# Optimization experiments

Measured on AMD Instinct MI355X. Metric: run time of the kernel, lower is better.

Reference implementation:

```python
import jax, jax.numpy as jnp
import numpy as np

B, N_MELS, T_IN = 4, 80, 2048
N_CTX, E, H, L, M, C = 1024, 768, 12, 6, 3072, 527
HD = E // H  # 64


def _sinusoids(length, channels, max_timescale=10000):
    log_inc = np.log(max_timescale) / (channels // 2 - 1)
    inv = np.exp(-log_inc * np.arange(channels // 2))
    t = np.arange(length)[:, None] * inv[None, :]
    return jnp.asarray(np.concatenate([np.sin(t), np.cos(t)], axis=1), dtype=jnp.float32)


def _ln(x, g, b, eps=1e-5):
    m = jnp.mean(x, axis=-1, keepdims=True)
    v = jnp.mean(jnp.square(x - m), axis=-1, keepdims=True)
    return (x - m) * jax.lax.rsqrt(v + eps) * g + b


def setup_inputs() -> dict:
    key = jax.random.key(0)
    ks = iter(jax.random.split(key, 40))
    s = 0.02
    d = {
        "x": jax.random.normal(next(ks), (B, N_MELS, T_IN), jnp.float32),
        "conv1_w": jax.random.normal(next(ks), (E, N_MELS, 3), jnp.float32) * s,
        "conv1_b": jnp.zeros((E,), jnp.float32),
        "conv2_w": jax.random.normal(next(ks), (E, E, 3), jnp.float32) * s,
        "conv2_b": jnp.zeros((E,), jnp.float32),
        "pos_emb": _sinusoids(N_CTX, E),
        "ln1_g": jnp.ones((L, E), jnp.float32),
        "ln1_b": jnp.zeros((L, E), jnp.float32),
        "wq": jax.random.normal(next(ks), (L, H, E, HD), jnp.float32) * s,
        "bq": jnp.zeros((L, H, HD), jnp.float32),
        "wk": jax.random.normal(next(ks), (L, H, E, HD), jnp.float32) * s,
        "bk": jnp.zeros((L, H, HD), jnp.float32),
        "wv": jax.random.normal(next(ks), (L, H, E, HD), jnp.float32) * s,
        "bv": jnp.zeros((L, H, HD), jnp.float32),
        "wo": jax.random.normal(next(ks), (L, E, E), jnp.float32) * s,
        "bo": jnp.zeros((L, E), jnp.float32),
        "w1": jax.random.normal(next(ks), (L, E, M), jnp.float32) * s,
        "b1": jnp.zeros((L, M), jnp.float32),
        "w2": jax.random.normal(next(ks), (L, M, E), jnp.float32) * s,
        "b2": jnp.zeros((L, E), jnp.float32),
        "ln2_g": jnp.ones((L, E), jnp.float32),
        "ln2_b": jnp.zeros((L, E), jnp.float32),
        "lnp_g": jnp.ones((E,), jnp.float32),
        "lnp_b": jnp.zeros((E,), jnp.float32),
        "hln_g": jnp.ones((E,), jnp.float32),
        "hln_b": jnp.zeros((E,), jnp.float32),
        "hw1": jax.random.normal(next(ks), (E, M), jnp.float32) * s,
        "hb1": jnp.zeros((M,), jnp.float32),
        "hw2": jax.random.normal(next(ks), (M, C), jnp.float32) * s,
        "hb2": jnp.zeros((C,), jnp.float32),
    }
    return d


def reference(x, conv1_w, conv1_b, conv2_w, conv2_b, pos_emb,
              ln1_g, ln1_b, wq, bq, wk, bk, wv, bv, wo, bo,
              w1, b1, w2, b2, ln2_g, ln2_b, lnp_g, lnp_b,
              hln_g, hln_b, hw1, hb1, hw2, hb2):
    # conv stem: (B, n_mels, T) -> (B, E, T) -> (B, E, T/2), exact (erf) GELU
    x = jax.lax.conv_general_dilated(x, conv1_w, (1,), [(1, 1)],
                                     dimension_numbers=("NCH", "OIH", "NCH"))
    x = jax.nn.gelu(x + conv1_b[None, :, None], approximate=False)
    x = jax.lax.conv_general_dilated(x, conv2_w, (2,), [(1, 1)],
                                     dimension_numbers=("NCH", "OIH", "NCH"))
    x = jax.nn.gelu(x + conv2_b[None, :, None], approximate=False)
    x = jnp.transpose(x, (0, 2, 1))  # (B, T, E), T == N_CTX
    x = x + pos_emb[: x.shape[1]]

    b, t, e = x.shape
    for l in range(L):
        # batched per-head QKV (original loops over heads; same math)
        q = jnp.einsum("bte,hed->bhtd", x, wq[l]) + bq[l][None, :, None, :]
        k = jnp.einsum("bte,hed->bhtd", x, wk[l]) + bk[l][None, :, None, :]
        v = jnp.einsum("bte,hed->bhtd", x, wv[l]) + bv[l][None, :, None, :]
        # NOTE: no 1/sqrt(d) scaling in the original module
        a = jax.nn.softmax(jnp.einsum("bhid,bhjd->bhij", q, k), axis=-1)
        hds = jnp.einsum("bhij,bhjd->bhid", a, v)
        concat = jnp.transpose(hds, (0, 2, 1, 3)).reshape(b, t, e)
        attn_out = concat @ wo[l] + bo[l]
        x = _ln(x + attn_out, ln1_g[l], ln1_b[l])
        ffn = jax.nn.relu(x @ w1[l] + b1[l]) @ w2[l] + b2[l]
        x = _ln(ffn + x, ln2_g[l], ln2_b[l])

    x = _ln(x, lnp_g, lnp_b)
    cls = x[:, 0]
    cls = _ln(cls, hln_g, hln_b)
    logits = jax.nn.relu(cls @ hw1 + hb1) @ hw2 + hb2  # dropout inactive (eval)
    return jax.nn.softmax(logits, axis=-1)
```

## Files before the change

kernel.cpp:

```cpp
#include <hip/hip_runtime.h>
#include <hip/hip_bf16.h>

typedef __hip_bfloat16 bf16;
using v8s   = __attribute__((ext_vector_type(8))) short;
using f32x4 = __attribute__((ext_vector_type(4))) float;

#define DI __device__ __forceinline__

DI float gelu_f(float x) { return 0.5f * x * (1.f + erff(x * 0.70710678118654752f)); }

DI void g2lds16(const bf16* g, bf16* l) {
  __builtin_amdgcn_global_load_lds((const __attribute__((address_space(1))) void*)g,
                                   (__attribute__((address_space(3))) void*)l, 16, 0, 0);
}

template<int N> DI void vm_barrier() {
  if constexpr (N == 0)      asm volatile("s_waitcnt vmcnt(0)\ns_barrier" ::: "memory");
  else if constexpr (N == 2) asm volatile("s_waitcnt vmcnt(2)\ns_barrier" ::: "memory");
  else if constexpr (N == 4) asm volatile("s_waitcnt vmcnt(4)\ns_barrier" ::: "memory");
  else if constexpr (N == 6) asm volatile("s_waitcnt vmcnt(6)\ns_barrier" ::: "memory");
  else if constexpr (N == 8) asm volatile("s_waitcnt vmcnt(8)\ns_barrier" ::: "memory");
}
DI void lds_barrier() { asm volatile("s_barrier" ::: "memory"); }

DI float block_sum(float v, float* red, int tid) {
#pragma unroll
  for (int o = 32; o > 0; o >>= 1) v += __shfl_down(v, o);
  __syncthreads();
  if ((tid & 63) == 0) red[tid >> 6] = v;
  __syncthreads();
  return red[0] + red[1] + red[2] + red[3];
}
DI float block_max(float v, float* red, int tid) {
#pragma unroll
  for (int o = 32; o > 0; o >>= 1) v = fmaxf(v, __shfl_down(v, o));
  __syncthreads();
  if ((tid & 63) == 0) red[tid >> 6] = v;
  __syncthreads();
  return fmaxf(fmaxf(red[0], red[1]), fmaxf(red[2], red[3]));
}

__global__ __launch_bounds__(256)
void tconv(const float* __restrict__ in, bf16* __restrict__ out,
           int R, int C, long inStrideZ, long outStrideL, long outStrideH, int zmod) {
  __shared__ float tile[32][33];
  int z = blockIdx.z;
  int lz = z / zmod, hz = z - lz * zmod;
  in  += (long)z * inStrideZ;
  out += (long)lz * outStrideL + (long)hz * outStrideH;
  int cb = blockIdx.x * 32, rb = blockIdx.y * 32;
  int tx = threadIdx.x & 31, ty = threadIdx.x >> 5;
#pragma unroll
  for (int i = 0; i < 32; i += 8)
    tile[ty + i][tx] = in[(long)(rb + ty + i) * C + cb + tx];
  __syncthreads();
#pragma unroll
  for (int i = 0; i < 32; i += 8)
    out[(long)(cb + ty + i) * R + rb + tx] = __float2bfloat16(tile[tx][ty + i]);
}

__global__ __launch_bounds__(256)
void prep_cw(const float* __restrict__ wsrc, bf16* __restrict__ o, int IC, int KT) {
  int idx = blockIdx.x * 256 + threadIdx.x;
  int oc = idx / KT, kp = idx - oc * KT;
  float v = 0.f;
  if (kp < IC * 3) {
    int kk = kp / IC, ic = kp - kk * IC;
    v = wsrc[(oc * IC + ic) * 3 + kk];
  }
  o[idx] = __float2bfloat16(v);
}

__global__ __launch_bounds__(256)
void prep_bias(const float* __restrict__ bq, const float* __restrict__ bk,
               const float* __restrict__ bv, float* __restrict__ o) {
  int idx = blockIdx.x * 256 + threadIdx.x;
  int l = idx / 2304, n = idx - l * 2304;
  int which = n / 768, r = n - which * 768;
  const float* src = which == 0 ? bq : (which == 1 ? bk : bv);
  o[idx] = src[l * 768 + r];
}

__global__ __launch_bounds__(256)
void prep_hw2(const float* __restrict__ hw2, const float* __restrict__ hb2,
              float* __restrict__ hw2p, float* __restrict__ hb2p) {
  int idx = blockIdx.x * 256 + threadIdx.x;
  int e = idx / 640, c = idx - e * 640;
  hw2p[idx] = c < 527 ? hw2[(long)e * 527 + c] : 0.f;
  if (idx < 640) hb2p[idx] = idx < 527 ? hb2[idx] : 0.f;
}

__global__ __launch_bounds__(256)
void im2col1(const float* __restrict__ x, bf16* __restrict__ out) {
  int idx = blockIdx.x * 256 + threadIdx.x;
  int m = idx >> 8, kp = idx & 255;
  float v = 0.f;
  if (kp < 240) {
    int kk = kp / 80, ic = kp - kk * 80;
    int t = (m & 2047) + kk - 1;
    int b = m >> 11;
    if ((unsigned)t < 2048u) v = x[((long)(b * 80 + ic) << 11) + t];
  }
  out[idx] = __float2bfloat16(v);
}

__global__ __launch_bounds__(256)
void im2col2(const bf16* __restrict__ y, bf16* __restrict__ out) {
  int idx = blockIdx.x * 256 + threadIdx.x;
  int m = idx / 2304, kp = idx - m * 2304;
  int kk = kp / 768, ic = kp - kk * 768;
  int t = 2 * (m & 1023) + kk - 1;
  bf16 v = __float2bfloat16(0.f);
  if ((unsigned)t < 2048u) v = y[((long)(m >> 10) * 2048 + t) * 768 + ic];
  out[idx] = v;
}

enum { EPI_GELU_BF16, EPI_CONV2, EPI_QKV, EPI_BIAS_F32, EPI_RELU_BF16 };

struct GP {
  const bf16* A; const bf16* B; const float* bias;
  bf16* Ob; float* Of; const float* aux;
  int M, N, K; long sA, sB, sC; int zoff;
};

template<int BM, int BN, int WM, int WN, int EPI, int DBUF>
__global__ __launch_bounds__(WM * WN * 64, 2)
void gemm_bt(GP p) {
  constexpr int WAVES = WM * WN;
  constexpr int FM = BM / WM / 16, FN = BN / WN / 16;
  constexpr int LDN = BM / 8 / WAVES + BN / 8 / WAVES;
  __shared__ __align__(16) bf16 As0[BM * 64], Bs0[BN * 64];
  __shared__ __align__(16) bf16 As1[DBUF ? BM * 64 : 8], Bs1[DBUF ? BN * 64 : 8];
  const int tid = threadIdx.x;
  const int lane = tid & 63, wid = tid >> 6;
  const int wr = wid / WN, wc = wid - wr * WN;
  const int row0 = wr * (BM / WM), col0 = wc * (BN / WN);
  const int lr = lane & 15, lk = (lane >> 4) * 8;
  const int lrow = lane >> 3;
  const int scol = (((lane & 7) ^ (lane >> 3)) & 7) * 8;
  const int rswz = (lr & 7) * 8;
  const int z = blockIdx.z;
  const bf16* Ab = p.A + (long)z * p.sA + (long)blockIdx.x * BM * p.K;
  const bf16* Bb = p.B + (long)z * p.sB + (long)blockIdx.y * BN * p.K;
  f32x4 acc[FM][FN] = {};

  auto stage = [&](bf16* As, bf16* Bs, int kt) {
#pragma unroll
    for (int i = 0; i < BM / 8 / WAVES; ++i) {
      const int c = wid + i * WAVES;
      g2lds16(&Ab[(long)(c * 8 + lrow) * p.K + kt + scol], &As[c << 9]);
    }
#pragma unroll
    for (int i = 0; i < BN / 8 / WAVES; ++i) {
      const int c = wid + i * WAVES;
      g2lds16(&Bb[(long)(c * 8 + lrow) * p.K + kt + scol], &Bs[c << 9]);
    }
  };

  auto compute = [&](const bf16* As, const bf16* Bs) {
#pragma unroll
    for (int ks = 0; ks < 2; ++ks) {
      v8s af[FM], bf_[FN];
#pragma unroll
      for (int mi = 0; mi < FM; ++mi)
        af[mi] = *(const v8s*)&As[(row0 + mi * 16 + lr) * 64 + ((ks * 32 + lk) ^ rswz)];
#pragma unroll
      for (int ni = 0; ni < FN; ++ni)
        bf_[ni] = *(const v8s*)&Bs[(col0 + ni * 16 + lr) * 64 + ((ks * 32 + lk) ^ rswz)];
      __builtin_amdgcn_s_setprio(1);
#pragma unroll
      for (int mi = 0; mi < FM; ++mi)
#pragma unroll
        for (int ni = 0; ni < FN; ++ni)
          acc[mi][ni] = __builtin_amdgcn_mfma_f32_16x16x32_bf16(af[mi], bf_[ni], acc[mi][ni], 0, 0, 0);
      __builtin_amdgcn_s_setprio(0);
    }
  };

  if constexpr (DBUF) {
    stage(As0, Bs0, 0);
    int kt = 0;
    while (true) {
      bool more = kt + 64 < p.K;
      if (more) { stage(As1, Bs1, kt + 64); vm_barrier<LDN>(); } else vm_barrier<0>();
      compute(As0, Bs0);
      kt += 64;
      if (kt >= p.K) break;
      lds_barrier();
      more = kt + 64 < p.K;
      if (more) { stage(As0, Bs0, kt + 64); vm_barrier<LDN>(); } else vm_barrier<0>();
      compute(As1, Bs1);
      kt += 64;
      if (kt >= p.K) break;
      lds_barrier();
    }
  } else {
    for (int kt = 0; kt < p.K; kt += 64) {
      __syncthreads();
      stage(As0, Bs0, kt);
      __syncthreads();
      compute(As0, Bs0);
    }
  }

#pragma unroll
  for (int mi = 0; mi < FM; ++mi) {
#pragma unroll
    for (int ni = 0; ni < FN; ++ni) {
#pragma unroll
      for (int r = 0; r < 4; ++r) {
        float v = acc[mi][ni][r];
        const int m = blockIdx.x * BM + row0 + mi * 16 + (lane >> 4) * 4 + r;
        const int n = blockIdx.y * BN + col0 + ni * 16 + lr;
        if constexpr (EPI == EPI_GELU_BF16) {
          p.Ob[(long)m * p.N + n] = __float2bfloat16(gelu_f(v + p.bias[n]));
        } else if constexpr (EPI == EPI_CONV2) {
          float t = gelu_f(v + p.bias[n]) + p.aux[(long)(m & 1023) * 768 + n];
          p.Of[(long)m * 768 + n] = t;
          p.Ob[(long)m * 768 + n] = __float2bfloat16(t);
        } else if constexpr (EPI == EPI_QKV) {
          float t = v + p.bias[n];
          int which = n / 768, nn = n - which * 768;
          int h = nn >> 6, d = nn & 63;
          long bh = (long)(m >> 10) * 12 + h;
          if (which < 2)
            p.Ob[(long)which * 3145728 + (bh << 16) + ((long)(m & 1023) << 6) + d] = __float2bfloat16(t);
          else
            p.Ob[6291456L + (bh << 16) + ((long)d << 10) + (m & 1023)] = __float2bfloat16(t);
        } else if constexpr (EPI == EPI_BIAS_F32) {
          p.Of[(long)m * p.N + n] = v + p.bias[n];
        } else if constexpr (EPI == EPI_RELU_BF16) {
          p.Ob[(long)m * p.N + n] = __float2bfloat16(fmaxf(v + p.bias[n], 0.f));
        }
      }
    }
  }
}

__global__ __launch_bounds__(256)
void attn_flash(const bf16* __restrict__ qkv, bf16* __restrict__ cc) {
  __shared__ __align__(16) bf16 Ks[2][64 * 64], Vs[2][64 * 64];
  __shared__ __align__(16) bf16 Pl[4][16 * 64];
  const int tid = threadIdx.x, lane = tid & 63, wid = tid >> 6;
  const int lr = lane & 15, lg = lane >> 4;
  const int blk = blockIdx.x;
  const int qt = blk / 48, bh = blk - qt * 48;
  const int b = bh / 12, h = bh - b * 12;
  const long qb = (long)bh << 16;
  const bf16* Qg = qkv + qb;
  const bf16* Kg = qkv + 3145728 + qb;
  const bf16* Vg = qkv + 6291456 + qb;
  const int q0 = qt * 64 + wid * 16;
  const int lrow8 = lane >> 3;
  const int scol = (((lane & 7) ^ (lane >> 3)) & 7) * 8;
  const int rswz = (lr & 7) * 8;

  v8s aq[2];
#pragma unroll
  for (int ks = 0; ks < 2; ++ks)
    aq[ks] = *(const v8s*)&Qg[(long)(q0 + lr) * 64 + ks * 32 + lg * 8];

  const short oneb = (short)0x3F80;
  const v8s ones = {oneb, oneb, oneb, oneb, oneb, oneb, oneb, oneb};

  float mrow[4] = {-1e30f, -1e30f, -1e30f, -1e30f};
  f32x4 acc[4] = {};
  f32x4 lacc = {};
  bf16* myP = &Pl[wid][0];

  auto stageKV = [&](int buf, int kt) {
#pragma unroll
    for (int i = 0; i < 2; ++i) {
      int c = wid + i * 4;
      g2lds16(&Kg[(long)(kt + c * 8 + lrow8) * 64 + scol], &Ks[buf][c << 9]);
      g2lds16(&Vg[((long)(c * 8 + lrow8) << 10) + kt + scol], &Vs[buf][c << 9]);
    }
  };

  stageKV(0, 0);

  for (int it = 0; it < 16; ++it) {
    const int cur = it & 1;
    if (it + 1 < 16) { stageKV(cur ^ 1, (it + 1) * 64); vm_barrier<4>(); }
    else vm_barrier<0>();
    const bf16* Kc = &Ks[cur][0];
    const bf16* Vc = &Vs[cur][0];

    f32x4 s[4] = {};
#pragma unroll
    for (int ks = 0; ks < 2; ++ks) {
      v8s bk[4];
#pragma unroll
      for (int ni = 0; ni < 4; ++ni)
        bk[ni] = *(const v8s*)&Kc[(ni * 16 + lr) * 64 + ((ks * 32 + lg * 8) ^ rswz)];
      __builtin_amdgcn_s_setprio(1);
#pragma unroll
      for (int ni = 0; ni < 4; ++ni)
        s[ni] = __builtin_amdgcn_mfma_f32_16x16x32_bf16(aq[ks], bk[ni], s[ni], 0, 0, 0);
      __builtin_amdgcn_s_setprio(0);
    }

    float tloc[4];
    bool need = false;
#pragma unroll
    for (int r = 0; r < 4; ++r) {
      tloc[r] = fmaxf(fmaxf(s[0][r], s[1][r]), fmaxf(s[2][r], s[3][r]));
      need = need || (tloc[r] > mrow[r] + 8.f);
    }
    if (__any(need)) {
#pragma unroll
      for (int r = 0; r < 4; ++r) {
        float t = tloc[r];
#pragma unroll
        for (int o = 1; o < 16; o <<= 1) t = fmaxf(t, __shfl_xor(t, o));
        float mn = fmaxf(mrow[r], t);
        float al = __expf(mrow[r] - mn);
        mrow[r] = mn;
        lacc[r] *= al;
#pragma unroll
        for (int ni = 0; ni < 4; ++ni) acc[ni][r] *= al;
      }
    }
#pragma unroll
    for (int r = 0; r < 4; ++r) {
      const int row = lg * 4 + r;
      const int prow = row * 64, psw = (row & 7) * 8;
#pragma unroll
      for (int ni = 0; ni < 4; ++ni)
        myP[prow + ((ni * 16 + lr) ^ psw)] = __float2bfloat16(__expf(s[ni][r] - mrow[r]));
    }

#pragma unroll
    for (int ks = 0; ks < 2; ++ks) {
      v8s pa, bv[4];
      pa = *(const v8s*)&myP[lr * 64 + ((ks * 32 + lg * 8) ^ ((lr & 7) * 8))];
#pragma unroll
      for (int ni = 0; ni < 4; ++ni)
        bv[ni] = *(const v8s*)&Vc[(ni * 16 + lr) * 64 + ((ks * 32 + lg * 8) ^ rswz)];
      __builtin_amdgcn_s_setprio(1);
#pragma unroll
      for (int ni = 0; ni < 4; ++ni)
        acc[ni] = __builtin_amdgcn_mfma_f32_16x16x32_bf16(pa, bv[ni], acc[ni], 0, 0, 0);
      lacc = __builtin_amdgcn_mfma_f32_16x16x32_bf16(pa, ones, lacc, 0, 0, 0);
      __builtin_amdgcn_s_setprio(0);
    }
    if (it < 15) lds_barrier();
  }

#pragma unroll
  for (int ni = 0; ni < 4; ++ni)
#pragma unroll
    for (int r = 0; r < 4; ++r) {
      int row = q0 + lg * 4 + r;
      cc[((long)(b << 10) + row) * 768 + h * 64 + ni * 16 + lr] =
          __float2bfloat16(acc[ni][r] / lacc[r]);
    }
}

__global__ __launch_bounds__(256)
void ln_resid(const float* __restrict__ xin, const float* __restrict__ add,
              const float* __restrict__ g, const float* __restrict__ bb,
              float* __restrict__ xo, bf16* __restrict__ xbo) {
  __shared__ float red[4];
  long row = blockIdx.x;
  int tid = threadIdx.x;
  const f32x4* xr = (const f32x4*)(xin + row * 768);
  const f32x4* ar = (const f32x4*)(add + row * 768);
  f32x4 v = {0.f, 0.f, 0.f, 0.f};
  if (tid < 192) {
    f32x4 a = xr[tid], c = ar[tid];
    v[0] = a[0] + c[0]; v[1] = a[1] + c[1]; v[2] = a[2] + c[2]; v[3] = a[3] + c[3];
  }
  float mean = block_sum(v[0] + v[1] + v[2] + v[3], red, tid) * (1.f / 768.f);
  if (tid < 192) { v[0] -= mean; v[1] -= mean; v[2] -= mean; v[3] -= mean; }
  float sq = tid < 192 ? v[0] * v[0] + v[1] * v[1] + v[2] * v[2] + v[3] * v[3] : 0.f;
  float var = block_sum(sq, red, tid) * (1.f / 768.f);
  float rs = rsqrtf(var + 1e-5f);
  if (tid < 192) {
    f32x4 gv = ((const f32x4*)g)[tid];
    f32x4 bv = ((const f32x4*)bb)[tid];
    f32x4 o;
    o[0] = v[0] * rs * gv[0] + bv[0];
    o[1] = v[1] * rs * gv[1] + bv[1];
    o[2] = v[2] * rs * gv[2] + bv[2];
    o[3] = v[3] * rs * gv[3] + bv[3];
    ((f32x4*)(xo + row * 768))[tid] = o;
    bf16 t0 = __float2bfloat16(o[0]), t1 = __float2bfloat16(o[1]);
    bf16 t2 = __float2bfloat16(o[2]), t3 = __float2bfloat16(o[3]);
    ushort4 pk;
    pk.x = *(unsigned short*)&t0; pk.y = *(unsigned short*)&t1;
    pk.z = *(unsigned short*)&t2; pk.w = *(unsigned short*)&t3;
    *(ushort4*)&xbo[row * 768 + tid * 4] = pk;
  }
}

__global__ __launch_bounds__(256)
void head_cls(const float* __restrict__ x,
              const float* __restrict__ lnpg, const float* __restrict__ lnpb,
              const float* __restrict__ hlng, const float* __restrict__ hlnb,
              float* __restrict__ cls) {
  __shared__ float red[4];
  int b = blockIdx.x, tid = threadIdx.x;
  const float* xr = x + (long)b * 1024 * 768;
  float v0 = xr[tid], v1 = xr[tid + 256], v2 = xr[tid + 512];
  float s = block_sum(v0 + v1 + v2, red, tid) * (1.f / 768.f);
  v0 -= s; v1 -= s; v2 -= s;
  float q = block_sum(v0 * v0 + v1 * v1 + v2 * v2, red, tid) * (1.f / 768.f);
  float r = rsqrtf(q + 1e-5f);
  v0 = v0 * r * lnpg[tid]       + lnpb[tid];
  v1 = v1 * r * lnpg[tid + 256] + lnpb[tid + 256];
  v2 = v2 * r * lnpg[tid + 512] + lnpb[tid + 512];
  s = block_sum(v0 + v1 + v2, red, tid) * (1.f / 768.f);
  v0 -= s; v1 -= s; v2 -= s;
  q = block_sum(v0 * v0 + v1 * v1 + v2 * v2, red, tid) * (1.f / 768.f);
  r = rsqrtf(q + 1e-5f);
  cls[b * 768 + tid]       = v0 * r * hlng[tid]       + hlnb[tid];
  cls[b * 768 + tid + 256] = v1 * r * hlng[tid + 256] + hlnb[tid + 256];
  cls[b * 768 + tid + 512] = v2 * r * hlng[tid + 512] + hlnb[tid + 512];
}

__global__ __launch_bounds__(256)
void mlp_part(const float* __restrict__ in, const float* __restrict__ wmat,
              float* __restrict__ part, int IN, int OUTP, int ET) {
  __shared__ float cin[4][96];
  __shared__ float red[8][32][16];
  int tid = threadIdx.x;
  int tx = tid & 31, ty = tid >> 5;
  int e0 = blockIdx.y * ET;
  for (int i = tid; i < 4 * ET; i += 256) {
    int b = i / ET, el = i - b * ET;
    cin[b][el] = in[b * IN + e0 + el];
  }
  __syncthreads();
  f32x4 acc[4] = {};
  const float* wp = wmat + (long)e0 * OUTP + (blockIdx.x * 32 + tx) * 4;
  const int iters = ET >> 3;
  for (int i = 0; i < iters; ++i) {
    int el = ty + i * 8;
    f32x4 w = *(const f32x4*)(wp + (long)el * OUTP);
#pragma unroll
    for (int b = 0; b < 4; ++b) acc[b] += cin[b][el] * w;
  }
#pragma unroll
  for (int b = 0; b < 4; ++b) *(f32x4*)&red[ty][tx][b * 4] = acc[b];
  __syncthreads();
  if (tid < 128) {
    int rx = tid & 31, b = tid >> 5;
    f32x4 s = {};
#pragma unroll
    for (int t = 0; t < 8; ++t) s += *(const f32x4*)&red[t][rx][b * 4];
    *(f32x4*)&part[((long)blockIdx.y * 4 + b) * OUTP + (blockIdx.x * 32 + rx) * 4] = s;
  }
}

__global__ __launch_bounds__(256)
void mlp_reduce(const float* __restrict__ part, const float* __restrict__ bias,
                float* __restrict__ out, int OUTP, int S, int relu) {
  int idx = blockIdx.x * 256 + threadIdx.x;
  int b = idx / OUTP, j = idx - b * OUTP;
  float s = bias[j];
  for (int t = 0; t < S; ++t) s += part[((long)t * 4 + b) * OUTP + j];
  out[idx] = relu ? fmaxf(s, 0.f) : s;
}

__global__ __launch_bounds__(256)
void head_softmax(const float* __restrict__ lg, float* __restrict__ out) {
  __shared__ float red[4];
  int b = blockIdx.x, tid = threadIdx.x;
  const float* r = lg + (long)b * 640;
  float v0 = r[tid];
  float v1 = tid + 256 < 527 ? r[tid + 256] : -1e30f;
  float v2 = tid + 512 < 527 ? r[tid + 512] : -1e30f;
  float mx = block_max(fmaxf(v0, fmaxf(v1, v2)), red, tid);
  float e0 = __expf(v0 - mx);
  float e1 = tid + 256 < 527 ? __expf(v1 - mx) : 0.f;
  float e2 = tid + 512 < 527 ? __expf(v2 - mx) : 0.f;
  float sm = block_sum(e0 + e1 + e2, red, tid);
  float inv = 1.f / sm;
  out[(long)b * 527 + tid] = e0 * inv;
  if (tid + 256 < 527) out[(long)b * 527 + tid + 256] = e1 * inv;
  if (tid + 512 < 527) out[(long)b * 527 + tid + 512] = e2 * inv;
}

extern "C" void kernel_launch(void* const* d_in, const int* in_sizes, int n_in,
                              void* d_out, int out_size, void* d_ws, size_t ws_size,
                              hipStream_t stream) {
  const float* x_in    = (const float*)d_in[0];
  const float* conv1_w = (const float*)d_in[1];
  const float* conv1_b = (const float*)d_in[2];
  const float* conv2_w = (const float*)d_in[3];
  const float* conv2_b = (const float*)d_in[4];
  const float* pos_emb = (const float*)d_in[5];
  const float* ln1_g   = (const float*)d_in[6];
  const float* ln1_b   = (const float*)d_in[7];
  const float* wq      = (const float*)d_in[8];
  const float* bq      = (const float*)d_in[9];
  const float* wk      = (const float*)d_in[10];
  const float* bk      = (const float*)d_in[11];
  const float* wv      = (const float*)d_in[12];
  const float* bv      = (const float*)d_in[13];
  const float* wo      = (const float*)d_in[14];
  const float* bo      = (const float*)d_in[15];
  const float* w1      = (const float*)d_in[16];
  const float* b1      = (const float*)d_in[17];
  const float* w2      = (const float*)d_in[18];
  const float* b2      = (const float*)d_in[19];
  const float* ln2_g   = (const float*)d_in[20];
  const float* ln2_b   = (const float*)d_in[21];
  const float* lnp_g   = (const float*)d_in[22];
  const float* lnp_b   = (const float*)d_in[23];
  const float* hln_g   = (const float*)d_in[24];
  const float* hln_b   = (const float*)d_in[25];
  const float* hw1     = (const float*)d_in[26];
  const float* hb1     = (const float*)d_in[27];
  const float* hw2     = (const float*)d_in[28];
  const float* hb2     = (const float*)d_in[29];

  char* w = (char*)d_ws;
  bf16*  wqkvT = (bf16*)(w);
  bf16*  woT   = (bf16*)(w + 21233664);
  bf16*  w1T   = (bf16*)(w + 28311552);
  bf16*  w2T   = (bf16*)(w + 56623104);
  bf16*  wc1T  = (bf16*)(w + 84934656);
  bf16*  wc2T  = (bf16*)(w + 85327872);
  float* bqkv  = (float*)(w + 88866816);
  float* Xf    = (float*)(w + 88922112);
  bf16*  Xb    = (bf16*)(w + 101505024);
  bf16*  qkv   = (bf16*)(w + 107796480);
  bf16*  CC    = (bf16*)(w + 126670848);
  float* ATTN  = (float*)(w + 132962304);
  char*  BIG   = w + 145545216;
  bf16*  A1  = (bf16*)(BIG);
  bf16*  Y1G = (bf16*)(BIG + 4194304);
  bf16*  A2  = (bf16*)(BIG + 16777216);
  bf16*  Hh  = (bf16*)(BIG);
  float* FFN = (float*)(BIG + 25165824);
  float* CLS  = (float*)(BIG);
  float* HID  = (float*)(BIG + 16384);
  float* LGT  = (float*)(BIG + 81920);
  float* PT1  = (float*)(BIG + 131072);
  float* PT2  = (float*)(BIG + 1048576);
  float* HB2P = (float*)(BIG + 1572864);
  float* HW2P = (float*)(BIG + 1605632);

  tconv<<<dim3(2, 24, 72), 256, 0, stream>>>(wq, wqkvT,            768, 64,   49152L, 1769472L, 49152L, 12);
  tconv<<<dim3(2, 24, 72), 256, 0, stream>>>(wk, wqkvT + 589824,   768, 64,   49152L, 1769472L, 49152L, 12);
  tconv<<<dim3(2, 24, 72), 256, 0, stream>>>(wv, wqkvT + 1179648,  768, 64,   49152L, 1769472L, 49152L, 12);
  tconv<<<dim3(24, 24, 6), 256, 0, stream>>>(wo, woT,              768, 768,  589824L, 589824L, 0L, 1);
  tconv<<<dim3(96, 24, 6), 256, 0, stream>>>(w1, w1T,              768, 3072, 2359296L, 2359296L, 0L, 1);
  tconv<<<dim3(24, 96, 6), 256, 0, stream>>>(w2, w2T,              3072, 768, 2359296L, 2359296L, 0L, 1);
  prep_cw<<<768,  256, 0, stream>>>(conv1_w, wc1T, 80, 256);
  prep_cw<<<6912, 256, 0, stream>>>(conv2_w, wc2T, 768, 2304);
  prep_bias<<<54, 256, 0, stream>>>(bq, bk, bv, bqkv);

  im2col1<<<8192, 256, 0, stream>>>(x_in, A1);
  { GP p{}; p.A = A1; p.B = wc1T; p.bias = conv1_b; p.Ob = Y1G;
    p.M = 8192; p.N = 768; p.K = 256;
    gemm_bt<128,64,2,2,EPI_GELU_BF16,1><<<dim3(64,12,1),256,0,stream>>>(p); }
  im2col2<<<36864, 256, 0, stream>>>(Y1G, A2);
  { GP p{}; p.A = A2; p.B = wc2T; p.bias = conv2_b; p.Of = Xf; p.Ob = Xb; p.aux = pos_emb;
    p.M = 4096; p.N = 768; p.K = 2304;
    gemm_bt<64,64,2,2,EPI_CONV2,1><<<dim3(64,12,1),256,0,stream>>>(p); }

  for (int l = 0; l < 6; ++l) {
    { GP p{}; p.A = Xb; p.B = wqkvT + (long)l * 1769472; p.bias = bqkv + l * 2304;
      p.Ob = qkv; p.M = 4096; p.N = 2304; p.K = 768;
      gemm_bt<128,128,2,2,EPI_QKV,0><<<dim3(32,18,1),256,0,stream>>>(p); }
    attn_flash<<<768, 256, 0, stream>>>(qkv, CC);
    { GP p{}; p.A = CC; p.B = woT + (long)l * 589824; p.bias = bo + l * 768; p.Of = ATTN;
      p.M = 4096; p.N = 768; p.K = 768;
      gemm_bt<64,64,2,2,EPI_BIAS_F32,1><<<dim3(64,12,1),256,0,stream>>>(p); }
    ln_resid<<<4096, 256, 0, stream>>>(Xf, ATTN, ln1_g + l * 768, ln1_b + l * 768, Xf, Xb);
    { GP p{}; p.A = Xb; p.B = w1T + (long)l * 2359296; p.bias = b1 + l * 3072; p.Ob = Hh;
      p.M = 4096; p.N = 3072; p.K = 768;
      gemm_bt<128,128,2,2,EPI_RELU_BF16,0><<<dim3(32,24,1),256,0,stream>>>(p); }
    { GP p{}; p.A = Hh; p.B = w2T + (long)l * 2359296; p.bias = b2 + l * 768; p.Of = FFN;
      p.M = 4096; p.N = 768; p.K = 3072;
      gemm_bt<64,64,2,2,EPI_BIAS_F32,1><<<dim3(64,12,1),256,0,stream>>>(p); }
    ln_resid<<<4096, 256, 0, stream>>>(Xf, FFN, ln2_g + l * 768, ln2_b + l * 768, Xf, Xb);
  }

  head_cls<<<4, 256, 0, stream>>>(Xf, lnp_g, lnp_b, hln_g, hln_b, CLS);
  prep_hw2<<<7680, 256, 0, stream>>>(hw2, hb2, HW2P, HB2P);
  mlp_part<<<dim3(24, 16), 256, 0, stream>>>(CLS, hw1, PT1, 768, 3072, 48);
  mlp_reduce<<<48, 256, 0, stream>>>(PT1, hb1, HID, 3072, 16, 1);
  mlp_part<<<dim3(5, 32), 256, 0, stream>>>(HID, HW2P, PT2, 3072, 640, 96);
  mlp_reduce<<<10, 256, 0, stream>>>(PT2, HB2P, LGT, 640, 32, 0);
  head_softmax<<<4, 256, 0, stream>>>(LGT, (float*)d_out);
}
```

Baseline: 1.081 ms.

## Generalize GEMM to multi-stage LDS pipeline and retile QKV/FFN1 to 128x96

Replaces the fixed double-buffer GEMM main loop with a ring buffer of configurable depth. Three stages are used for the conv2, output-projection and FFN2 GEMMs so more global-to-LDS loads are in flight while the current tile computes. The QKV and FFN1 GEMMs move from 128x128 to 128x96 tiles, giving more blocks for better CU fill. Deeper buffering costs more LDS per block, which may reduce occupancy, and the narrower tiles lower data reuse per block.

Result: slower. 1.121 ms (+3.6%).

```diff
diff --git a/kernel.cpp b/kernel.cpp
--- a/kernel.cpp
+++ b/kernel.cpp
@@ -15,11 +15,12 @@
 }
 
 template<int N> DI void vm_barrier() {
-  if constexpr (N == 0)      asm volatile("s_waitcnt vmcnt(0)\ns_barrier" ::: "memory");
-  else if constexpr (N == 2) asm volatile("s_waitcnt vmcnt(2)\ns_barrier" ::: "memory");
-  else if constexpr (N == 4) asm volatile("s_waitcnt vmcnt(4)\ns_barrier" ::: "memory");
-  else if constexpr (N == 6) asm volatile("s_waitcnt vmcnt(6)\ns_barrier" ::: "memory");
-  else if constexpr (N == 8) asm volatile("s_waitcnt vmcnt(8)\ns_barrier" ::: "memory");
+  if constexpr (N == 0)       asm volatile("s_waitcnt vmcnt(0)\ns_barrier" ::: "memory");
+  else if constexpr (N == 2)  asm volatile("s_waitcnt vmcnt(2)\ns_barrier" ::: "memory");
+  else if constexpr (N == 4)  asm volatile("s_waitcnt vmcnt(4)\ns_barrier" ::: "memory");
+  else if constexpr (N == 6)  asm volatile("s_waitcnt vmcnt(6)\ns_barrier" ::: "memory");
+  else if constexpr (N == 8)  asm volatile("s_waitcnt vmcnt(8)\ns_barrier" ::: "memory");
+  else if constexpr (N == 12) asm volatile("s_waitcnt vmcnt(12)\ns_barrier" ::: "memory");
 }
 DI void lds_barrier() { asm volatile("s_barrier" ::: "memory"); }
 
@@ -123,14 +124,15 @@
   int M, N, K; long sA, sB, sC; int zoff;
 };
 
-template<int BM, int BN, int WM, int WN, int EPI, int DBUF>
+template<int BM, int BN, int WM, int WN, int EPI, int DEPTH>
 __global__ __launch_bounds__(WM * WN * 64, 2)
 void gemm_bt(GP p) {
   constexpr int WAVES = WM * WN;
   constexpr int FM = BM / WM / 16, FN = BN / WN / 16;
   constexpr int LDN = BM / 8 / WAVES + BN / 8 / WAVES;
-  __shared__ __align__(16) bf16 As0[BM * 64], Bs0[BN * 64];
-  __shared__ __align__(16) bf16 As1[DBUF ? BM * 64 : 8], Bs1[DBUF ? BN * 64 : 8];
+  constexpr int NB = DEPTH ? DEPTH : 1;
+  __shared__ __align__(16) bf16 AsBuf[NB * BM * 64];
+  __shared__ __align__(16) bf16 BsBuf[NB * BN * 64];
   const int tid = threadIdx.x;
   const int lane = tid & 63, wid = tid >> 6;
   const int wr = wid / WN, wc = wid - wr * WN;
@@ -177,29 +179,31 @@
     }
   };
 
-  if constexpr (DBUF) {
-    stage(As0, Bs0, 0);
-    int kt = 0;
-    while (true) {
-      bool more = kt + 64 < p.K;
-      if (more) { stage(As1, Bs1, kt + 64); vm_barrier<LDN>(); } else vm_barrier<0>();
-      compute(As0, Bs0);
-      kt += 64;
-      if (kt >= p.K) break;
-      lds_barrier();
-      more = kt + 64 < p.K;
-      if (more) { stage(As0, Bs0, kt + 64); vm_barrier<LDN>(); } else vm_barrier<0>();
-      compute(As1, Bs1);
-      kt += 64;
-      if (kt >= p.K) break;
-      lds_barrier();
-    }
-  } else {
+  if constexpr (DEPTH == 0) {
     for (int kt = 0; kt < p.K; kt += 64) {
       __syncthreads();
-      stage(As0, Bs0, kt);
+      stage(AsBuf, BsBuf, kt);
       __syncthreads();
-      compute(As0, Bs0);
+      compute(AsBuf, BsBuf);
+    }
+  } else {
+    const int nt = p.K >> 6;
+#pragma unroll
+    for (int i = 0; i < DEPTH - 1; ++i)
+      stage(AsBuf + i * BM * 64, BsBuf + i * BN * 64, i * 64);
+    int cur = 0, aidx = DEPTH - 1;
+    for (int t = 0; t < nt; ++t) {
+      const int ahead = t + DEPTH - 1;
+      if (ahead < nt) {
+        stage(AsBuf + aidx * BM * 64, BsBuf + aidx * BN * 64, ahead * 64);
+        vm_barrier<(DEPTH - 1) * LDN>();
+      } else {
+        vm_barrier<0>();
+      }
+      compute(AsBuf + cur * BM * 64, BsBuf + cur * BN * 64);
+      cur = (cur + 1 == DEPTH) ? 0 : cur + 1;
+      aidx = (aidx + 1 == DEPTH) ? 0 : aidx + 1;
+      if (t + 1 < nt) lds_barrier();
     }
   }
 
@@ -556,27 +560,27 @@
   im2col1<<<8192, 256, 0, stream>>>(x_in, A1);
   { GP p{}; p.A = A1; p.B = wc1T; p.bias = conv1_b; p.Ob = Y1G;
     p.M = 8192; p.N = 768; p.K = 256;
-    gemm_bt<128,64,2,2,EPI_GELU_BF16,1><<<dim3(64,12,1),256,0,stream>>>(p); }
+    gemm_bt<128,64,2,2,EPI_GELU_BF16,2><<<dim3(64,12,1),256,0,stream>>>(p); }
   im2col2<<<36864, 256, 0, stream>>>(Y1G, A2);
   { GP p{}; p.A = A2; p.B = wc2T; p.bias = conv2_b; p.Of = Xf; p.Ob = Xb; p.aux = pos_emb;
     p.M = 4096; p.N = 768; p.K = 2304;
-    gemm_bt<64,64,2,2,EPI_CONV2,1><<<dim3(64,12,1),256,0,stream>>>(p); }
+    gemm_bt<64,64,2,2,EPI_CONV2,3><<<dim3(64,12,1),256,0,stream>>>(p); }
 
   for (int l = 0; l < 6; ++l) {
     { GP p{}; p.A = Xb; p.B = wqkvT + (long)l * 1769472; p.bias = bqkv + l * 2304;
       p.Ob = qkv; p.M = 4096; p.N = 2304; p.K = 768;
-      gemm_bt<128,128,2,2,EPI_QKV,0><<<dim3(32,18,1),256,0,stream>>>(p); }
+      gemm_bt<128,96,2,2,EPI_QKV,0><<<dim3(32,24,1),256,0,stream>>>(p); }
     attn_flash<<<768, 256, 0, stream>>>(qkv, CC);
     { GP p{}; p.A = CC; p.B = woT + (long)l * 589824; p.bias = bo + l * 768; p.Of = ATTN;
       p.M = 4096; p.N = 768; p.K = 768;
-      gemm_bt<64,64,2,2,EPI_BIAS_F32,1><<<dim3(64,12,1),256,0,stream>>>(p); }
+      gemm_bt<64,64,2,2,EPI_BIAS_F32,3><<<dim3(64,12,1),256,0,stream>>>(p); }
     ln_resid<<<4096, 256, 0, stream>>>(Xf, ATTN, ln1_g + l * 768, ln1_b + l * 768, Xf, Xb);
     { GP p{}; p.A = Xb; p.B = w1T + (long)l * 2359296; p.bias = b1 + l * 3072; p.Ob = Hh;
       p.M = 4096; p.N = 3072; p.K = 768;
-      gemm_bt<128,128,2,2,EPI_RELU_BF16,0><<<dim3(32,24,1),256,0,stream>>>(p); }
+      gemm_bt<128,96,2,2,EPI_RELU_BF16,0><<<dim3(32,32,1),256,0,stream>>>(p); }
     { GP p{}; p.A = Hh; p.B = w2T + (long)l * 2359296; p.bias = b2 + l * 768; p.Of = FFN;
       p.M = 4096; p.N = 768; p.K = 3072;
-      gemm_bt<64,64,2,2,EPI_BIAS_F32,1><<<dim3(64,12,1),256,0,stream>>>(p); }
+      gemm_bt<64,64,2,2,EPI_BIAS_F32,3><<<dim3(64,12,1),256,0,stream>>>(p); }
     ln_resid<<<4096, 256, 0, stream>>>(Xf, FFN, ln2_g + l * 768, ln2_b + l * 768, Xf, Xb);
   }
 
```
